# Kernel tuning notes

Hardware: AMD Instinct MI355X
Metric: run time of the kernel (lower is better)

## Reference

```python
import jax, jax.numpy as jnp
import numpy as np
from jax import lax

B, T, D, H = 32, 2048, 512, 512


def setup_inputs() -> dict:
    key = jax.random.key(0)
    k1, k2, k3 = jax.random.split(key, 3)
    inputs = jax.random.normal(k1, (B, T, D), dtype=jnp.float32)
    input_paddings = jnp.zeros((B, T), dtype=jnp.float32)  # all tokens valid
    c0 = jnp.zeros((B, H), dtype=jnp.float32)
    h0 = jnp.zeros((B, H), dtype=jnp.float32)
    # flax LSTMCell params fused: dense_i kernel [D,4H] (no bias), dense_h kernel [H,4H] + bias [4H]
    Wi = jax.random.normal(k2, (D, 4 * H), dtype=jnp.float32) * 0.05
    Wh = jax.random.normal(k3, (H, 4 * H), dtype=jnp.float32) * 0.05
    b = jnp.zeros((4 * H,), dtype=jnp.float32)
    return {"inputs": inputs, "input_paddings": input_paddings,
            "c0": c0, "h0": h0, "Wi": Wi, "Wh": Wh, "b": b}


def reference(inputs, input_paddings, c0, h0, Wi, Wh, b):
    # reverse=False path: lengths are computed but unused.
    del input_paddings
    # Precompute input projections for all timesteps in one big GEMM: [B,T,4H]
    x_proj = jnp.einsum('btd,dg->btg', inputs, Wi)

    def step(carry, xp_t):
        c, h = carry
        z = xp_t + h @ Wh + b  # [B, 4H]
        i, f, g, o = jnp.split(z, 4, axis=-1)  # flax gate order: i, f, g, o
        c_new = jax.nn.sigmoid(f) * c + jax.nn.sigmoid(i) * jnp.tanh(g)
        h_new = jax.nn.sigmoid(o) * jnp.tanh(c_new)
        return (c_new, h_new), h_new

    xs = jnp.swapaxes(x_proj, 0, 1)  # [T, B, 4H]
    _, outs = lax.scan(step, (c0, h0), xs)
    return jnp.swapaxes(outs, 0, 1)  # [B, T, H]
```

## Files before the change

kernel.cpp:

```cpp
#include <hip/hip_runtime.h>
#include <cstdint>
#include <cstddef>

#define TT 2048
#define DD 512

#define BM 128
#define BN 128
#define BK 16

__global__ __launch_bounds__(256) void xproj_gemm(
    const float* __restrict__ A,
    const float* __restrict__ W,
    const float* __restrict__ bias,
    float* __restrict__ C,
    int t0, int tmask, int tlog)
{
    __shared__ __align__(16) float As[BK][BM + 4];
    __shared__ __align__(16) float Bs[BK][BN + 4];
    const int tid = threadIdx.x;
    const int nt = blockIdx.x;
    const int mt = blockIdx.y;
    const int m_base = mt * BM;
    const int n_base = nt * BN;
    const int ty = tid >> 4;
    const int tx = tid & 15;

    float acc[8][8];
#pragma unroll
    for (int i = 0; i < 8; ++i)
#pragma unroll
        for (int j = 0; j < 8; ++j) acc[i][j] = 0.f;

    for (int k0 = 0; k0 < DD; k0 += BK) {
#pragma unroll
        for (int j = 0; j < 2; ++j) {
            int idx = tid * 2 + j;
            int rowl = idx >> 2, q = idx & 3;
            int rc = m_base + rowl;
            int rg = ((rc >> tlog) << 11) + t0 + (rc & tmask);
            float4 av = *(const float4*)(A + (size_t)rg * DD + k0 + q * 4);
            As[q * 4 + 0][rowl] = av.x;
            As[q * 4 + 1][rowl] = av.y;
            As[q * 4 + 2][rowl] = av.z;
            As[q * 4 + 3][rowl] = av.w;
            int kr = idx >> 5, nq = idx & 31;
            *(float4*)&Bs[kr][nq * 4] =
                *(const float4*)(W + (size_t)(k0 + kr) * 2048 + n_base + nq * 4);
        }
        __syncthreads();
#pragma unroll
        for (int kk = 0; kk < BK; ++kk) {
            float a[8], bb[8];
            *(float4*)&a[0]  = *(const float4*)&As[kk][ty * 8];
            *(float4*)&a[4]  = *(const float4*)&As[kk][ty * 8 + 4];
            *(float4*)&bb[0] = *(const float4*)&Bs[kk][tx * 8];
            *(float4*)&bb[4] = *(const float4*)&Bs[kk][tx * 8 + 4];
#pragma unroll
            for (int i = 0; i < 8; ++i)
#pragma unroll
                for (int j = 0; j < 8; ++j)
                    acc[i][j] = fmaf(a[i], bb[j], acc[i][j]);
        }
        __syncthreads();
    }
#pragma unroll
    for (int i = 0; i < 8; ++i) {
        int m = m_base + ty * 8 + i;
        int bglob = m >> tlog, tl = m & tmask;
#pragma unroll
        for (int j = 0; j < 8; j += 4) {
            int n = n_base + tx * 8 + j;
            int gate = n >> 9, c = n & 511;
            float4 v;
            v.x = acc[i][j + 0] + bias[n + 0];
            v.y = acc[i][j + 1] + bias[n + 1];
            v.z = acc[i][j + 2] + bias[n + 2];
            v.w = acc[i][j + 3] + bias[n + 3];
            size_t addr = (((size_t)tl * 4 + gate) * 32 + bglob) * 512 + c;
            *(float4*)(C + addr) = v;
        }
    }
}

#define NGRP 8
#define BPG  32
#define HSZ  (32 * 512)
#define POISON 0xFFFFFFFFu
#define WHST 516

__device__ __forceinline__ float ldg_agent_f32(const float* p) {
    return __hip_atomic_load(p, __ATOMIC_RELAXED, __HIP_MEMORY_SCOPE_AGENT);
}

template<int CTRL>
__device__ __forceinline__ float dppf(float x) {
    return __int_as_float(
        __builtin_amdgcn_update_dpp(0, __float_as_int(x), CTRL, 0xf, 0xf, true));
}

__device__ __forceinline__ void soft_bar(unsigned* ctr, bool leader, unsigned target) {
    asm volatile("s_waitcnt lgkmcnt(0)" ::: "memory");
    if (leader)
        __hip_atomic_fetch_add(ctr, 1u, __ATOMIC_RELAXED, __HIP_MEMORY_SCOPE_WORKGROUP);
    while (__hip_atomic_load(ctr, __ATOMIC_RELAXED, __HIP_MEMORY_SCOPE_WORKGROUP) < target)
        __builtin_amdgcn_s_sleep(1);
    __builtin_amdgcn_sched_barrier(0);
}

template<int D, int HALF>
__device__ __forceinline__ void rstep(float* p, int lane) {
    const bool hi = (lane & D) != 0;
#pragma unroll
    for (int i = 0; i < HALF; ++i) {
        float send = hi ? p[i] : p[i + HALF];
        float recv;
        if constexpr (D == 1)      recv = dppf<0xB1>(send);
        else if constexpr (D == 2) recv = dppf<0x4E>(send);
        else                       recv = __shfl_xor(send, D, 64);
        p[i] = (hi ? p[i + HALF] : p[i]) + recv;
    }
}

__global__ __launch_bounds__(512) void lstm_scan(
    const float* __restrict__ xp,
    const float* __restrict__ Wh,
    const float* __restrict__ c0,
    const float* __restrict__ h0,
    float* __restrict__ out,
    float* hbuf,
    float* __restrict__ cbuf,
    int t0, int T_CH)
{
    __shared__ float wh[64 * WHST];
    __shared__ float hs[2 * 4 * 512];
    __shared__ unsigned scnt;

    const int tid  = threadIdx.x;
    const int blk  = blockIdx.x;
    const int g    = blk >> 5;
    const int p    = blk & 31;
    const int j0   = p * 16;
    const int lane = tid & 63;
    const int w    = tid >> 6;

    const int idx = ((lane & 1) << 4) | ((lane & 2) << 2) | (lane & 4)
                  | ((lane >> 2) & 2) | ((lane >> 4) & 1);
    const int gate = idx >> 3;
    const int cc   = (idx >> 2) & 1;
    const int bq   = idx & 3;
    const int B    = 4 * g + bq;
    const int col  = j0 + 2 * w + cc;
    const bool low = lane < 32;
    const bool act = low && ((lane & 3) == 0);

    if (tid == 0) scnt = 0u;

    float creg = 0.f;
    if (act) {
        size_t o = (size_t)B * 512 + col;
        if (t0 == 0) {
            creg = c0[o];
            float hv = h0[o];
            if (__float_as_uint(hv) == POISON) hv = __uint_as_float(0xFFFFFFFEu);
            __hip_atomic_store(hbuf + o, hv, __ATOMIC_RELAXED, __HIP_MEMORY_SCOPE_AGENT);
        } else {
            creg = cbuf[o];
        }
    }

#pragma unroll
    for (int i = 0; i < 16; ++i) {
        int id = tid + i * 512;
        int q4 = id & 3, gt = (id >> 2) & 3, k = id >> 4;
        float4 v = *(const float4*)(Wh + (size_t)k * 2048 + gt * 512 + j0 + q4 * 4);
        int r0 = gt * 16 + q4 * 4;
        wh[(r0 + 0) * WHST + k] = v.x;
        wh[(r0 + 1) * WHST + k] = v.y;
        wh[(r0 + 2) * WHST + k] = v.z;
        wh[(r0 + 3) * WHST + k] = v.w;
    }

    const int sb = w >> 1;
    const int sh = (w & 1) * 256;

    float xr = 0.f, xn = 0.f;
    if (low) xr = xp[((size_t)gate * 32 + B) * 512 + col];

    __syncthreads();

    unsigned starget = 0;

    for (int tl = 0; tl < T_CH; ++tl) {
        const int t = t0 + tl;
        const int cur = t % 3;
        const int nxt = (t + 1) % 3;
        const int rcy = (t + 2) % 3;

        if (low && (tl + 1 < T_CH))
            xn = xp[((size_t)((tl + 1) * 4 + gate) * 32 + B) * 512 + col];

        const float* hsrc = hbuf + (size_t)cur * HSZ
                          + (size_t)(4 * g + sb) * 512 + sh + lane;
        float hvv[4];
        for (;;) {
            bool ok = true;
#pragma unroll
            for (int q = 0; q < 4; ++q) {
                hvv[q] = ldg_agent_f32(hsrc + q * 64);
                ok = ok & (__float_as_uint(hvv[q]) != POISON);
            }
            if (ok) break;
            __builtin_amdgcn_s_sleep(1);
        }
        float* hdst = hs + (tl & 1) * 2048 + sb * 512 + sh + lane;
#pragma unroll
        for (int q = 0; q < 4; ++q) hdst[q * 64] = hvv[q];

        starget += 8;
        soft_bar(&scnt, lane == 0, starget);

        if (act)
            __hip_atomic_store(hbuf + (size_t)rcy * HSZ + (size_t)B * 512 + col,
                               __uint_as_float(POISON),
                               __ATOMIC_RELAXED, __HIP_MEMORY_SCOPE_AGENT);
        asm volatile("" ::: "memory");

        const float* hb = hs + (tl & 1) * 2048;
        float4 ha[4], h2[4];
#pragma unroll
        for (int b = 0; b < 4; ++b) {
            ha[b] = *(const float4*)(hb + b * 512 + 4 * lane);
            h2[b] = *(const float4*)(hb + b * 512 + 256 + 4 * lane);
        }
        float pp[32];
#pragma unroll
        for (int i = 0; i < 32; ++i) pp[i] = 0.f;
#pragma unroll
        for (int gt = 0; gt < 4; ++gt)
#pragma unroll
            for (int c2 = 0; c2 < 2; ++c2) {
                const float* wr = wh + (size_t)(gt * 16 + 2 * w + c2) * WHST + 4 * lane;
                float4 w0 = *(const float4*)wr;
                float4 w1 = *(const float4*)(wr + 256);
#pragma unroll
                for (int b = 0; b < 4; ++b) {
                    float a = pp[gt * 8 + c2 * 4 + b];
                    a = fmaf(ha[b].x, w0.x, a);
                    a = fmaf(ha[b].y, w0.y, a);
                    a = fmaf(ha[b].z, w0.z, a);
                    a = fmaf(ha[b].w, w0.w, a);
                    a = fmaf(h2[b].x, w1.x, a);
                    a = fmaf(h2[b].y, w1.y, a);
                    a = fmaf(h2[b].z, w1.z, a);
                    a = fmaf(h2[b].w, w1.w, a);
                    pp[gt * 8 + c2 * 4 + b] = a;
                }
            }

        rstep<1, 16>(pp, lane);
        rstep<2, 8>(pp, lane);
        rstep<4, 4>(pp, lane);
        rstep<8, 2>(pp, lane);
        rstep<16, 1>(pp, lane);
        float v0 = pp[0] + __shfl_xor(pp[0], 32, 64);

        float av = 0.f;
        if (low) {
            float zz = v0 + xr;
            av = (gate == 2) ? tanhf(zz) : 1.f / (1.f + expf(-zz));
        }
        float ag = dppf<0xB1>(av);
        float af = dppf<0x4E>(av);
        float ao = dppf<0x1B>(av);

        float hn = 0.f;
        if (act) {
            float cn = af * creg + av * ag;
            hn = ao * tanhf(cn);
            creg = cn;
            __hip_atomic_store(hbuf + (size_t)nxt * HSZ + (size_t)B * 512 + col,
                               hn, __ATOMIC_RELAXED, __HIP_MEMORY_SCOPE_AGENT);
            out[((size_t)B * TT + t) * 512 + col] = hn;
        }
        if (low) xr = xn;
    }

    if (act) cbuf[(size_t)B * 512 + col] = creg;
}

extern "C" void kernel_launch(void* const* d_in, const int* in_sizes, int n_in,
                              void* d_out, int out_size, void* d_ws, size_t ws_size,
                              hipStream_t stream) {
    const float* inputs = (const float*)d_in[0];
    const float* c0   = (const float*)d_in[2];
    const float* h0   = (const float*)d_in[3];
    const float* Wi   = (const float*)d_in[4];
    const float* Wh   = (const float*)d_in[5];
    const float* bias = (const float*)d_in[6];
    float* out = (float*)d_out;

    float* ws_f = (float*)d_ws;
    float* hbuf = ws_f;
    float* cbuf = ws_f + 3 * HSZ;
    float* xp   = ws_f + 4 * HSZ;
    const size_t extras_bytes = (size_t)(4 * HSZ) * sizeof(float);

    int T_CH = 256;
    while (T_CH > 32 &&
           extras_bytes + (size_t)T_CH * 65536 * sizeof(float) > ws_size)
        T_CH >>= 1;
    int tlog = 31 - __builtin_clz((unsigned)T_CH);

    hipMemsetAsync(hbuf, 0xFF, (size_t)(3 * HSZ) * sizeof(float), stream);

    for (int t0 = 0; t0 < TT; t0 += T_CH) {
        dim3 g1(2048 / BN, (32 * T_CH) / BM);
        xproj_gemm<<<g1, 256, 0, stream>>>(inputs, Wi, bias, xp, t0, T_CH - 1, tlog);

        const float* xp_c = xp;
        int t0_arg = t0, tch_arg = T_CH;
        void* args[] = { (void*)&xp_c, (void*)&Wh, (void*)&c0, (void*)&h0,
                         (void*)&out, (void*)&hbuf, (void*)&cbuf,
                         (void*)&t0_arg, (void*)&tch_arg };
        hipLaunchCooperativeKernel((const void*)lstm_scan, dim3(NGRP * BPG), dim3(512),
                                   args, 0, stream);
    }
}
```

Measured before the change: 7.721 ms.

## Interleave h in LDS for packed FMA, pipeline poll loads, enlarge time chunk

Stores the hidden-state tile in LDS with pairs of batch rows interleaved, so the recurrent matvec can use packed two-wide FMAs (v_pk_fma_f32) with a broadcast weight. The spin-wait on h now keeps two rounds of loads in flight so polling latency overlaps. The next-step xp prefetch moves after the barrier, and the time-chunk size doubles to 512 to halve the number of GEMM/scan launch pairs. It adds register pressure and a larger workspace requirement, and the chunk size still falls back if the workspace is too small.

```diff
diff --git a/kernel.cpp b/kernel.cpp
--- a/kernel.cpp
+++ b/kernel.cpp
@@ -89,8 +89,13 @@
 #define POISON 0xFFFFFFFFu
 #define WHST 516
 
+typedef float v2f __attribute__((ext_vector_type(2)));
+
 __device__ __forceinline__ float ldg_agent_f32(const float* p) {
     return __hip_atomic_load(p, __ATOMIC_RELAXED, __HIP_MEMORY_SCOPE_AGENT);
+}
+__device__ __forceinline__ v2f fma2(v2f a, v2f b, v2f c) {
+    return __builtin_elementwise_fma(a, b, c);
 }
 
 template<int CTRL>
@@ -133,7 +138,7 @@
     int t0, int T_CH)
 {
     __shared__ float wh[64 * WHST];
-    __shared__ float hs[2 * 4 * 512];
+    __shared__ float hs2[2 * 2048];
     __shared__ unsigned scnt;
 
     const int tid  = threadIdx.x;
@@ -183,6 +188,8 @@
 
     const int sb = w >> 1;
     const int sh = (w & 1) * 256;
+    const int sp = sb >> 1;
+    const int se = sb & 1;
 
     float xr = 0.f, xn = 0.f;
     if (low) xr = xp[((size_t)gate * 32 + B) * 512 + col];
@@ -197,25 +204,42 @@
         const int nxt = (t + 1) % 3;
         const int rcy = (t + 2) % 3;
 
-        if (low && (tl + 1 < T_CH))
-            xn = xp[((size_t)((tl + 1) * 4 + gate) * 32 + B) * 512 + col];
-
         const float* hsrc = hbuf + (size_t)cur * HSZ
                           + (size_t)(4 * g + sb) * 512 + sh + lane;
-        float hvv[4];
-        for (;;) {
-            bool ok = true;
-#pragma unroll
-            for (int q = 0; q < 4; ++q) {
-                hvv[q] = ldg_agent_f32(hsrc + q * 64);
-                ok = ok & (__float_as_uint(hvv[q]) != POISON);
+        float hvv0, hvv1, hvv2, hvv3;
+        {
+            float a0 = ldg_agent_f32(hsrc);
+            float a1 = ldg_agent_f32(hsrc + 64);
+            float a2 = ldg_agent_f32(hsrc + 128);
+            float a3 = ldg_agent_f32(hsrc + 192);
+            for (;;) {
+                float b0 = ldg_agent_f32(hsrc);
+                float b1 = ldg_agent_f32(hsrc + 64);
+                float b2 = ldg_agent_f32(hsrc + 128);
+                float b3 = ldg_agent_f32(hsrc + 192);
+                if ((__float_as_uint(a0) != POISON) & (__float_as_uint(a1) != POISON) &
+                    (__float_as_uint(a2) != POISON) & (__float_as_uint(a3) != POISON)) {
+                    hvv0 = a0; hvv1 = a1; hvv2 = a2; hvv3 = a3; break;
+                }
+                __builtin_amdgcn_s_sleep(1);
+                a0 = ldg_agent_f32(hsrc);
+                a1 = ldg_agent_f32(hsrc + 64);
+                a2 = ldg_agent_f32(hsrc + 128);
+                a3 = ldg_agent_f32(hsrc + 192);
+                if ((__float_as_uint(b0) != POISON) & (__float_as_uint(b1) != POISON) &
+                    (__float_as_uint(b2) != POISON) & (__float_as_uint(b3) != POISON)) {
+                    hvv0 = b0; hvv1 = b1; hvv2 = b2; hvv3 = b3; break;
+                }
+                __builtin_amdgcn_s_sleep(1);
             }
-            if (ok) break;
-            __builtin_amdgcn_s_sleep(1);
-        }
-        float* hdst = hs + (tl & 1) * 2048 + sb * 512 + sh + lane;
-#pragma unroll
-        for (int q = 0; q < 4; ++q) hdst[q * 64] = hvv[q];
+        }
+        {
+            float* hd = hs2 + (tl & 1) * 2048 + sp * 1024 + 2 * (sh + lane) + se;
+            hd[0]       = hvv0;
+            hd[2 * 64]  = hvv1;
+            hd[2 * 128] = hvv2;
+            hd[2 * 192] = hvv3;
+        }
 
         starget += 8;
         soft_bar(&scnt, lane == 0, starget);
@@ -226,16 +250,22 @@
                                __ATOMIC_RELAXED, __HIP_MEMORY_SCOPE_AGENT);
         asm volatile("" ::: "memory");
 
-        const float* hb = hs + (tl & 1) * 2048;
-        float4 ha[4], h2[4];
-#pragma unroll
-        for (int b = 0; b < 4; ++b) {
-            ha[b] = *(const float4*)(hb + b * 512 + 4 * lane);
-            h2[b] = *(const float4*)(hb + b * 512 + 256 + 4 * lane);
-        }
-        float pp[32];
-#pragma unroll
-        for (int i = 0; i < 32; ++i) pp[i] = 0.f;
+        if (low && (tl + 1 < T_CH))
+            xn = xp[((size_t)((tl + 1) * 4 + gate) * 32 + B) * 512 + col];
+
+        const float* hb2 = hs2 + (tl & 1) * 2048;
+        float4 hq[2][4];
+#pragma unroll
+        for (int pp_ = 0; pp_ < 2; ++pp_) {
+            const float* hp2 = hb2 + pp_ * 1024 + 8 * lane;
+            hq[pp_][0] = *(const float4*)(hp2);
+            hq[pp_][1] = *(const float4*)(hp2 + 4);
+            hq[pp_][2] = *(const float4*)(hp2 + 512);
+            hq[pp_][3] = *(const float4*)(hp2 + 516);
+        }
+        v2f acc2[16];
+#pragma unroll
+        for (int i = 0; i < 16; ++i) acc2[i] = (v2f)(0.f);
 #pragma unroll
         for (int gt = 0; gt < 4; ++gt)
 #pragma unroll
@@ -244,19 +274,29 @@
                 float4 w0 = *(const float4*)wr;
                 float4 w1 = *(const float4*)(wr + 256);
 #pragma unroll
-                for (int b = 0; b < 4; ++b) {
-                    float a = pp[gt * 8 + c2 * 4 + b];
-                    a = fmaf(ha[b].x, w0.x, a);
-                    a = fmaf(ha[b].y, w0.y, a);
-                    a = fmaf(ha[b].z, w0.z, a);
-                    a = fmaf(ha[b].w, w0.w, a);
-                    a = fmaf(h2[b].x, w1.x, a);
-                    a = fmaf(h2[b].y, w1.y, a);
-                    a = fmaf(h2[b].z, w1.z, a);
-                    a = fmaf(h2[b].w, w1.w, a);
-                    pp[gt * 8 + c2 * 4 + b] = a;
+                for (int pq = 0; pq < 2; ++pq) {
+                    v2f a = acc2[gt * 4 + c2 * 2 + pq];
+                    a = fma2((v2f){hq[pq][0].x, hq[pq][0].y}, (v2f){w0.x, w0.x}, a);
+                    a = fma2((v2f){hq[pq][0].z, hq[pq][0].w}, (v2f){w0.y, w0.y}, a);
+                    a = fma2((v2f){hq[pq][1].x, hq[pq][1].y}, (v2f){w0.z, w0.z}, a);
+                    a = fma2((v2f){hq[pq][1].z, hq[pq][1].w}, (v2f){w0.w, w0.w}, a);
+                    a = fma2((v2f){hq[pq][2].x, hq[pq][2].y}, (v2f){w1.x, w1.x}, a);
+                    a = fma2((v2f){hq[pq][2].z, hq[pq][2].w}, (v2f){w1.y, w1.y}, a);
+                    a = fma2((v2f){hq[pq][3].x, hq[pq][3].y}, (v2f){w1.z, w1.z}, a);
+                    a = fma2((v2f){hq[pq][3].z, hq[pq][3].w}, (v2f){w1.w, w1.w}, a);
+                    acc2[gt * 4 + c2 * 2 + pq] = a;
                 }
             }
+        float pp[32];
+#pragma unroll
+        for (int gt = 0; gt < 4; ++gt)
+#pragma unroll
+            for (int c2 = 0; c2 < 2; ++c2)
+#pragma unroll
+                for (int pq = 0; pq < 2; ++pq) {
+                    pp[gt * 8 + c2 * 4 + 2 * pq + 0] = acc2[gt * 4 + c2 * 2 + pq].x;
+                    pp[gt * 8 + c2 * 4 + 2 * pq + 1] = acc2[gt * 4 + c2 * 2 + pq].y;
+                }
 
         rstep<1, 16>(pp, lane);
         rstep<2, 8>(pp, lane);
@@ -306,7 +346,7 @@
     float* xp   = ws_f + 4 * HSZ;
     const size_t extras_bytes = (size_t)(4 * HSZ) * sizeof(float);
 
-    int T_CH = 256;
+    int T_CH = 512;
     while (T_CH > 32 &&
            extras_bytes + (size_t)T_CH * 65536 * sizeof(float) > ws_size)
         T_CH >>= 1;
```

Measured after the change: 15.53 ms. 101% more time.
